# Optimization experiments

Measured on AMD Instinct MI355X. Metric: run time of the kernel, lower is better.

The kernel has to match this reference:

```python
import jax, jax.numpy as jnp
import numpy as np

N, E, G = 200000, 600000, 1024
NF_IN, EF_IN, H = 32, 16, 512
BN_EPS = 1e-5


def _bn(x, gamma, beta):
    # eval-mode BatchNorm1d with running_mean=0, running_var=1
    return x * (gamma / jnp.sqrt(1.0 + BN_EPS)) + beta


def setup_inputs() -> dict:
    key = jax.random.key(0)
    ks = jax.random.split(key, 32)
    s = 0.05
    inp = {
        'nf': jax.random.normal(ks[0], (N, NF_IN), jnp.float32),
        'ef': jax.random.normal(ks[1], (E, EF_IN), jnp.float32),
        'gf': jax.random.normal(ks[2], (G, H), jnp.float32),
        'device_params': jax.random.uniform(ks[3], (N,), jnp.float32),
        'node_y': jax.random.randint(ks[4], (N,), 0, 9),
        'batch_idx': jnp.sort(jax.random.randint(ks[5], (N,), 0, G)),
        'edge_index': jax.random.randint(ks[6], (2, E), 0, N),
        'nf_w1': jax.random.normal(ks[7], (NF_IN + 9, H), jnp.float32) * s,
        'nf_b1': jax.random.normal(ks[8], (H,), jnp.float32) * s,
        'nf_g1': jax.random.uniform(ks[9], (H,), jnp.float32, 0.5, 1.5),
        'nf_be1': jax.random.normal(ks[10], (H,), jnp.float32) * s,
        'nf_w2': jax.random.normal(ks[11], (H, H), jnp.float32) * s,
        'nf_b2': jax.random.normal(ks[12], (H,), jnp.float32) * s,
        'ef_w1': jax.random.normal(ks[13], (EF_IN, H), jnp.float32) * s,
        'ef_b1': jax.random.normal(ks[14], (H,), jnp.float32) * s,
        'ef_g1': jax.random.uniform(ks[15], (H,), jnp.float32, 0.5, 1.5),
        'ef_be1': jax.random.normal(ks[16], (H,), jnp.float32) * s,
        'ef_w2': jax.random.normal(ks[17], (H, H), jnp.float32) * s,
        'ef_b2': jax.random.normal(ks[18], (H,), jnp.float32) * s,
        'ow1': jax.random.normal(ks[19], (H, H), jnp.float32) * s,
        'ob1': jax.random.normal(ks[20], (H,), jnp.float32) * s,
        'og1': jax.random.uniform(ks[21], (H,), jnp.float32, 0.5, 1.5),
        'obe1': jax.random.normal(ks[22], (H,), jnp.float32) * s,
        'ow2': jax.random.normal(ks[23], (H, H), jnp.float32) * s,
        'ob2': jax.random.normal(ks[24], (H,), jnp.float32) * s,
        'og2': jax.random.uniform(ks[25], (H,), jnp.float32, 0.5, 1.5),
        'obe2': jax.random.normal(ks[26], (H,), jnp.float32) * s,
        'ow3': jax.random.normal(ks[27], (H, 2), jnp.float32) * s,
        'ob3': jax.random.normal(ks[28], (2,), jnp.float32) * s,
    }
    return inp


def reference(nf, ef, gf, device_params, node_y, batch_idx, edge_index,
              nf_w1, nf_b1, nf_g1, nf_be1, nf_w2, nf_b2,
              ef_w1, ef_b1, ef_g1, ef_be1, ef_w2, ef_b2,
              ow1, ob1, og1, obe1, ow2, ob2, og2, obe2, ow3, ob3):
    num_graphs = gf.shape[0]
    gelu = lambda x: jax.nn.gelu(x, approximate=False)  # torch nn.GELU default

    # DeviceParam_MLP: augment node features with scaled one-hot of node class
    nf_aug = jnp.concatenate(
        [nf, jax.nn.one_hot(node_y, 9, dtype=nf.dtype) * device_params[:, None]],
        axis=-1)  # [N, nf_in+9]
    h_n = gelu(_bn(nf_aug @ nf_w1 + nf_b1, nf_g1, nf_be1)) @ nf_w2 + nf_b2  # [N,H]
    h_e = gelu(_bn(ef @ ef_w1 + ef_b1, ef_g1, ef_be1)) @ ef_w2 + ef_b2      # [E,H]

    # two scatter_add pools into graph features
    gh = gf
    gh = gh + jax.ops.segment_sum(h_n, batch_idx, num_segments=num_graphs)
    edge_graph = batch_idx[edge_index[0]]  # graph id of each edge's source node
    gh = gh + jax.ops.segment_sum(h_e, edge_graph, num_segments=num_graphs)

    # output MLP (layer_num=3): two hidden blocks + final Linear -> 2
    x = gelu(_bn(gh @ ow1 + ob1, og1, obe1))
    x = gelu(_bn(x @ ow2 + ob2, og2, obe2))
    return x @ ow3 + ob3  # [G, 2]
```

## Files before the change

### kernel.cpp

```cpp
#include <hip/hip_runtime.h>

#define NN 200000
#define NE 600000
#define NG 1024
#define HH 512

typedef short short8 __attribute__((ext_vector_type(8)));
typedef float f32x4 __attribute__((ext_vector_type(4)));
typedef unsigned short ushort_t;

__device__ __forceinline__ unsigned short f2bf(float f){
  unsigned u = __float_as_uint(f);
  u += 0x7fffu + ((u >> 16) & 1u);
  return (unsigned short)(u >> 16);
}
__device__ __forceinline__ float bf2f(unsigned short h){
  return __uint_as_float(((unsigned)h) << 16);
}

__device__ __forceinline__ float gelu_f(float x){
  float p = __builtin_fmaf(x*x, -0.10294325f, -2.3022085f);
  float e = __builtin_amdgcn_exp2f(x * p);
  return x * __builtin_amdgcn_rcpf(1.0f + e);
}

__global__ __launch_bounds__(256) void kpre(
    const float* __restrict__ nfw1, const float* __restrict__ nfb1,
    const float* __restrict__ nfg1, const float* __restrict__ nfbe1,
    const float* __restrict__ efw1, const float* __restrict__ efb1,
    const float* __restrict__ efg1, const float* __restrict__ efbe1,
    unsigned short* __restrict__ w1nT, unsigned short* __restrict__ w1eT,
    float* __restrict__ b1n, float* __restrict__ b1e,
    const int* __restrict__ bidx, int* __restrict__ nstart,
    const int* __restrict__ eidx, int* __restrict__ eg, int* __restrict__ cnte,
    const float* __restrict__ w2n, const float* __restrict__ w2e,
    const float* __restrict__ ow1, const float* __restrict__ ow2,
    ushort_t* __restrict__ bt1h, ushort_t* __restrict__ bt1l,
    ushort_t* __restrict__ bt2h, ushort_t* __restrict__ bt2l,
    ushort_t* __restrict__ bt3h, ushort_t* __restrict__ bt3l){
  __shared__ int h[NG];
  const float rs = 0.99999500003750f;
  int b = blockIdx.x, t = threadIdx.x;
  if (b < 196){
    int tid = b*256 + t;
    if (tid < 512*64){
      int c = tid >> 6, k = tid & 63;
      float w = (k < 41) ? nfw1[k*HH + c] * nfg1[c] * rs : 0.0f;
      w1nT[tid] = f2bf(w);
    } else if (tid < 512*96){
      int u = tid - 512*64; int c = u >> 5, k = u & 31;
      float w = (k < 16) ? efw1[k*HH + c] * efg1[c] * rs : 0.0f;
      w1eT[u] = f2bf(w);
    } else if (tid < 512*96 + 512){
      int c = tid - 512*96;
      b1n[c] = nfb1[c]*nfg1[c]*rs + nfbe1[c];
    } else if (tid < 512*96 + 1024){
      int c = tid - (512*96 + 512);
      b1e[c] = efb1[c]*efg1[c]*rs + efbe1[c];
    }
  } else if (b < 978){
    int i = (b-196)*256 + t;
    if (i < NN){
      int g0 = bidx[i];
      int g1 = (i+1 < NN) ? bidx[i+1] : NG;
      for (int g = g0+1; g <= g1; ++g) nstart[g] = i+1;
      if (i == 0) for (int g = 0; g <= g0; ++g) nstart[g] = 0;
    }
  } else if (b < 1234){
    int hb = b - 978;
    for (int u = t; u < NG; u += 256) h[u] = 0;
    __syncthreads();
    for (int e = hb*256 + t; e < NE; e += 256*256){
      int g = bidx[eidx[e]];
      eg[e] = g;
      atomicAdd(&h[g], 1);
    }
    __syncthreads();
    for (int u = t; u < NG; u += 256){ int c = h[u]; if (c) atomicAdd(&cnte[u], c); }
  } else if (b < 3282){
    int u = (b - 1234)*256 + t;
    int c = u >> 10, k = u & 1023;
    float w = (k < HH) ? w2n[k*HH + c] : w2e[(k-HH)*HH + c];
    unsigned short hh = f2bf(w);
    bt1h[u] = hh;
    bt1l[u] = f2bf(w - bf2f(hh));
  } else if (b < 4306){
    int u = (b - 3282)*256 + t;
    int c = u >> 9, k = u & 511;
    float w = ow1[k*HH + c];
    unsigned short hh = f2bf(w);
    bt2h[u] = hh;
    bt2l[u] = f2bf(w - bf2f(hh));
  } else {
    int u = (b - 4306)*256 + t;
    int c = u >> 9, k = u & 511;
    float w = ow2[k*HH + c];
    unsigned short hh = f2bf(w);
    bt3h[u] = hh;
    bt3l[u] = f2bf(w - bf2f(hh));
  }
}

__global__ __launch_bounds__(1024) void kscan_init(const int* __restrict__ cnte, int* __restrict__ cursor,
    int* __restrict__ estart,
    const float* __restrict__ gf, const int* __restrict__ nstart,
    const float* __restrict__ b2n, const float* __restrict__ b2e,
    float* __restrict__ gh){
  if (blockIdx.x == 0){
    __shared__ int s[NG];
    int t = threadIdx.x;
    int v = cnte[t]; s[t] = v; __syncthreads();
    for (int d = 1; d < NG; d <<= 1){
      int x = (t >= d) ? s[t-d] : 0;
      __syncthreads();
      s[t] += x;
      __syncthreads();
    }
    cursor[t] = s[t] - v;
    estart[t] = s[t] - v;
    if (t == NG-1) estart[NG] = s[t];
  } else {
    int i = (blockIdx.x - 1)*1024 + threadIdx.x;
    int f = i*4;
    int r = f >> 9, c = f & 511;
    float cn = (float)(nstart[r+1] - nstart[r]);
    float ce = (float)cnte[r];
    float4 gv = *(const float4*)&gf[f];
    float4 bn4 = *(const float4*)&b2n[c];
    float4 be4 = *(const float4*)&b2e[c];
    float4 o;
    o.x = gv.x + cn*bn4.x + ce*be4.x;
    o.y = gv.y + cn*bn4.y + ce*be4.y;
    o.z = gv.z + cn*bn4.z + ce*be4.z;
    o.w = gv.w + cn*bn4.w + ce*be4.w;
    *(float4*)&gh[f] = o;
  }
}

__global__ __launch_bounds__(1024) void kscatter(const int* __restrict__ eg, int* __restrict__ cursor,
                                                 int* __restrict__ perm){
  __shared__ int h[NG], base[NG];
  const int per = (NE + gridDim.x - 1) / gridDim.x;
  const int lo = blockIdx.x * per, hi = min(lo + per, NE);
  for (int t = threadIdx.x; t < NG; t += 1024) h[t] = 0;
  __syncthreads();
  for (int e = lo + threadIdx.x; e < hi; e += 1024) atomicAdd(&h[eg[e]], 1);
  __syncthreads();
  for (int t = threadIdx.x; t < NG; t += 1024){
    int c = h[t];
    base[t] = c ? atomicAdd(&cursor[t], c) : 0;
    h[t] = 0;
  }
  __syncthreads();
  for (int e = lo + threadIdx.x; e < hi; e += 1024){
    int g = eg[e];
    int p = base[g] + atomicAdd(&h[g], 1);
    perm[p] = e;
  }
}

__global__ __launch_bounds__(256) void kmain(
    const float* __restrict__ nf, const float* __restrict__ dp, const int* __restrict__ ny,
    const int* __restrict__ nstart, const float* __restrict__ ef, const int* __restrict__ perm,
    const int* __restrict__ estart, const unsigned short* __restrict__ w1nT,
    const unsigned short* __restrict__ w1eT, const float* __restrict__ b1n,
    const float* __restrict__ b1e, float* __restrict__ S){
  const int t = threadIdx.x;
  const int lane = t & 63, w = t >> 6;
  const int q = lane >> 4, m = lane & 15;
  const short8 zz = {0,0,0,0,0,0,0,0};
  if (blockIdx.x < 2048){
    const int g = blockIdx.x >> 1;
    const int c0 = ((blockIdx.x & 1) << 8) + (w << 6);
    short8 bfr[4]; float bias[4]; float colacc[4] = {0.f,0.f,0.f,0.f};
#pragma unroll
    for (int nt=0; nt<4; ++nt){
      int c = c0 + (nt<<4) + m;
      bfr[nt] = *(const short8*)(w1eT + (c << 5) + (q << 3));
      bias[nt] = b1e[c];
    }
    const int s0 = estart[g], s1 = estart[g+1];
    const int nfull = (s1 - s0) >> 4;
    int rb = s0;
    for (int ch=0; ch<nfull; ++ch, rb += 16){
      int e = perm[rb + m];
      short8 f = zz;
      if (q < 2){
        const float4* ap = (const float4*)(ef + (size_t)e*16 + (q<<3));
        float4 xa = ap[0], xb = ap[1];
        f[0]=(short)f2bf(xa.x); f[1]=(short)f2bf(xa.y); f[2]=(short)f2bf(xa.z); f[3]=(short)f2bf(xa.w);
        f[4]=(short)f2bf(xb.x); f[5]=(short)f2bf(xb.y); f[6]=(short)f2bf(xb.z); f[7]=(short)f2bf(xb.w);
      }
#pragma unroll
      for (int nt=0; nt<4; ++nt){
        f32x4 acc = {bias[nt], bias[nt], bias[nt], bias[nt]};
        acc = __builtin_amdgcn_mfma_f32_16x16x32_bf16(f, bfr[nt], acc, 0, 0, 0);
        colacc[nt] += (gelu_f(acc[0]) + gelu_f(acc[1])) + (gelu_f(acc[2]) + gelu_f(acc[3]));
      }
    }
    if (rb < s1){
      int row = rb + m;
      int e = perm[(row < s1) ? row : s0];
      short8 f = zz;
      if (q < 2){
        const float4* ap = (const float4*)(ef + (size_t)e*16 + (q<<3));
        float4 xa = ap[0], xb = ap[1];
        f[0]=(short)f2bf(xa.x); f[1]=(short)f2bf(xa.y); f[2]=(short)f2bf(xa.z); f[3]=(short)f2bf(xa.w);
        f[4]=(short)f2bf(xb.x); f[5]=(short)f2bf(xb.y); f[6]=(short)f2bf(xb.z); f[7]=(short)f2bf(xb.w);
      }
      const int vr = s1 - rb;
#pragma unroll
      for (int nt=0; nt<4; ++nt){
        f32x4 acc = {bias[nt], bias[nt], bias[nt], bias[nt]};
        acc = __builtin_amdgcn_mfma_f32_16x16x32_bf16(f, bfr[nt], acc, 0, 0, 0);
        float v0 = (q*4+0 < vr) ? gelu_f(acc[0]) : 0.f;
        float v1 = (q*4+1 < vr) ? gelu_f(acc[1]) : 0.f;
        float v2 = (q*4+2 < vr) ? gelu_f(acc[2]) : 0.f;
        float v3 = (q*4+3 < vr) ? gelu_f(acc[3]) : 0.f;
        colacc[nt] += (v0+v1)+(v2+v3);
      }
    }
#pragma unroll
    for (int nt=0; nt<4; ++nt){
      float s = colacc[nt];
      s += __shfl_xor(s, 16); s += __shfl_xor(s, 32);
      if (lane < 16) S[(size_t)g*1024 + 512 + c0 + (nt<<4) + lane] = s;
    }
  } else {
    const int b2 = blockIdx.x - 2048;
    const int g = b2 >> 2;
    const int c0 = ((b2 & 3) << 7) + (w << 5);
    short8 bf0[2], bf1[2]; float bias[2]; float colacc[2] = {0.f,0.f};
#pragma unroll
    for (int nt=0; nt<2; ++nt){
      int c = c0 + (nt<<4) + m;
      const short8* bp = (const short8*)(w1nT + (c << 6) + (q << 3));
      bf0[nt] = bp[0]; bf1[nt] = bp[4];
      bias[nt] = b1n[c];
    }
    const int s0 = nstart[g], s1 = nstart[g+1];
    const int nfull = (s1 - s0) >> 4;
    int rb = s0;
    for (int ch=0; ch<nfull; ++ch, rb += 16){
      int ar = rb + m;
      const float4* ap = (const float4*)(nf + (size_t)ar*32 + (q<<3));
      float4 xa = ap[0], xb = ap[1];
      short8 f;
      f[0]=(short)f2bf(xa.x); f[1]=(short)f2bf(xa.y); f[2]=(short)f2bf(xa.z); f[3]=(short)f2bf(xa.w);
      f[4]=(short)f2bf(xb.x); f[5]=(short)f2bf(xb.y); f[6]=(short)f2bf(xb.z); f[7]=(short)f2bf(xb.w);
      int cls = ny[ar];
      short dpb = (short)f2bf(dp[ar]);
      short8 h = zz;
      if (q == 0){
#pragma unroll
        for (int j=0;j<8;++j) h[j] = (cls==j) ? dpb : (short)0;
      } else if (q == 1 && cls == 8) h[0] = dpb;
#pragma unroll
      for (int nt=0; nt<2; ++nt){
        f32x4 acc = {bias[nt], bias[nt], bias[nt], bias[nt]};
        acc = __builtin_amdgcn_mfma_f32_16x16x32_bf16(f, bf0[nt], acc, 0, 0, 0);
        acc = __builtin_amdgcn_mfma_f32_16x16x32_bf16(h, bf1[nt], acc, 0, 0, 0);
        colacc[nt] += (gelu_f(acc[0]) + gelu_f(acc[1])) + (gelu_f(acc[2]) + gelu_f(acc[3]));
      }
    }
    if (rb < s1){
      int row = rb + m;
      int ar = (row < s1) ? row : s0;
      const float4* ap = (const float4*)(nf + (size_t)ar*32 + (q<<3));
      float4 xa = ap[0], xb = ap[1];
      short8 f;
      f[0]=(short)f2bf(xa.x); f[1]=(short)f2bf(xa.y); f[2]=(short)f2bf(xa.z); f[3]=(short)f2bf(xa.w);
      f[4]=(short)f2bf(xb.x); f[5]=(short)f2bf(xb.y); f[6]=(short)f2bf(xb.z); f[7]=(short)f2bf(xb.w);
      int cls = ny[ar];
      short dpb = (short)f2bf(dp[ar]);
      short8 h = zz;
      if (q == 0){
#pragma unroll
        for (int j=0;j<8;++j) h[j] = (cls==j) ? dpb : (short)0;
      } else if (q == 1 && cls == 8) h[0] = dpb;
      const int vr = s1 - rb;
#pragma unroll
      for (int nt=0; nt<2; ++nt){
        f32x4 acc = {bias[nt], bias[nt], bias[nt], bias[nt]};
        acc = __builtin_amdgcn_mfma_f32_16x16x32_bf16(f, bf0[nt], acc, 0, 0, 0);
        acc = __builtin_amdgcn_mfma_f32_16x16x32_bf16(h, bf1[nt], acc, 0, 0, 0);
        float v0 = (q*4+0 < vr) ? gelu_f(acc[0]) : 0.f;
        float v1 = (q*4+1 < vr) ? gelu_f(acc[1]) : 0.f;
        float v2 = (q*4+2 < vr) ? gelu_f(acc[2]) : 0.f;
        float v3 = (q*4+3 < vr) ? gelu_f(acc[3]) : 0.f;
        colacc[nt] += (v0+v1)+(v2+v3);
      }
    }
#pragma unroll
    for (int nt=0; nt<2; ++nt){
      float s = colacc[nt];
      s += __shfl_xor(s, 16); s += __shfl_xor(s, 32);
      if (lane < 16) S[(size_t)g*1024 + c0 + (nt<<4) + lane] = s;
    }
  }
}

__global__ __launch_bounds__(256) void kgemm2(const float* __restrict__ A, int lda, int nkc,
    const ushort_t* __restrict__ bth, const ushort_t* __restrict__ btl, int ldb,
    float* __restrict__ out, const float* __restrict__ pre, const float* __restrict__ bias,
    const float* __restrict__ gam, const float* __restrict__ bet){
  const int t = threadIdx.x, lane = t & 63, w = t >> 6;
  const int q = lane >> 4, m = lane & 15;
  const int c0 = blockIdx.x*32, r0 = blockIdx.y*64 + w*16;
  f32x4 acc[2] = {{0.f,0.f,0.f,0.f},{0.f,0.f,0.f,0.f}};
  const float* ap = A + (size_t)(r0 + m)*lda + (q<<3);
  const ushort_t* bh0 = bth + (size_t)(c0 + m)*ldb + (q<<3);
  const ushort_t* bl0 = btl + (size_t)(c0 + m)*ldb + (q<<3);
  for (int kc = 0; kc < nkc; ++kc){
    const int ko = kc*32;
    float4 x = *(const float4*)(ap + ko);
    float4 y = *(const float4*)(ap + ko + 4);
    float v[8] = {x.x,x.y,x.z,x.w,y.x,y.y,y.z,y.w};
    short8 ah, al;
#pragma unroll
    for (int j=0;j<8;++j){
      unsigned short hh = f2bf(v[j]);
      ah[j] = (short)hh;
      al[j] = (short)f2bf(v[j] - bf2f(hh));
    }
#pragma unroll
    for (int cf=0; cf<2; ++cf){
      short8 bh = *(const short8*)(bh0 + (size_t)(cf*16)*ldb + ko);
      short8 bl = *(const short8*)(bl0 + (size_t)(cf*16)*ldb + ko);
      acc[cf] = __builtin_amdgcn_mfma_f32_16x16x32_bf16(ah, bh, acc[cf], 0, 0, 0);
      acc[cf] = __builtin_amdgcn_mfma_f32_16x16x32_bf16(ah, bl, acc[cf], 0, 0, 0);
      acc[cf] = __builtin_amdgcn_mfma_f32_16x16x32_bf16(al, bh, acc[cf], 0, 0, 0);
    }
  }
  const float rs = 0.99999500003750f;
#pragma unroll
  for (int cf=0; cf<2; ++cf){
    int c = c0 + cf*16 + m;
    float sc = 0.f, bi = 0.f, be = 0.f;
    if (!pre){ sc = gam[c]*rs; bi = bias[c]; be = bet[c]; }
#pragma unroll
    for (int i=0;i<4;++i){
      int r = blockIdx.y*64 + w*16 + q*4 + i;
      float vv = acc[cf][i];
      if (pre) vv += pre[(size_t)r*HH + c];
      else vv = gelu_f((vv + bi)*sc + be);
      out[(size_t)r*HH + c] = vv;
    }
  }
}

__global__ __launch_bounds__(256) void kfinal(const float* __restrict__ x2, const float* __restrict__ w3,
    const float* __restrict__ b3, float* __restrict__ out){
  const int lane = threadIdx.x & 63, wv = threadIdx.x >> 6;
  const int r = blockIdx.x*4 + wv;
  float a0 = 0.f, a1 = 0.f;
#pragma unroll
  for (int tt=0; tt<8; ++tt){
    int k = lane + tt*64;
    float x = x2[(size_t)r*HH + k];
    a0 = __builtin_fmaf(x, w3[2*k], a0);
    a1 = __builtin_fmaf(x, w3[2*k+1], a1);
  }
#pragma unroll
  for (int d=1; d<64; d<<=1){ a0 += __shfl_xor(a0, d); a1 += __shfl_xor(a1, d); }
  if (lane == 0){ out[r*2] = a0 + b3[0]; out[r*2+1] = a1 + b3[1]; }
}

extern "C" void kernel_launch(void* const* d_in, const int* in_sizes, int n_in,
                              void* d_out, int out_size, void* d_ws, size_t ws_size,
                              hipStream_t stream) {
  const float* nf    = (const float*)d_in[0];
  const float* ef    = (const float*)d_in[1];
  const float* gf    = (const float*)d_in[2];
  const float* dp    = (const float*)d_in[3];
  const int*   ny    = (const int*)d_in[4];
  const int*   bidx  = (const int*)d_in[5];
  const int*   eidx  = (const int*)d_in[6];
  const float* nfw1  = (const float*)d_in[7];
  const float* nfb1  = (const float*)d_in[8];
  const float* nfg1  = (const float*)d_in[9];
  const float* nfbe1 = (const float*)d_in[10];
  const float* w2n   = (const float*)d_in[11];
  const float* b2n   = (const float*)d_in[12];
  const float* efw1  = (const float*)d_in[13];
  const float* efb1  = (const float*)d_in[14];
  const float* efg1  = (const float*)d_in[15];
  const float* efbe1 = (const float*)d_in[16];
  const float* w2e   = (const float*)d_in[17];
  const float* b2e   = (const float*)d_in[18];
  const float* ow1   = (const float*)d_in[19];
  const float* ob1   = (const float*)d_in[20];
  const float* og1   = (const float*)d_in[21];
  const float* obe1  = (const float*)d_in[22];
  const float* ow2   = (const float*)d_in[23];
  const float* ob2   = (const float*)d_in[24];
  const float* og2   = (const float*)d_in[25];
  const float* obe2  = (const float*)d_in[26];
  const float* ow3   = (const float*)d_in[27];
  const float* ob3   = (const float*)d_in[28];

  float* S    = (float*)d_ws;
  int* cnte   = (int*)(S + NG*1024);
  int* cursor = cnte + NG;
  int* nstart = cursor + NG;
  int* estart = nstart + NG + 1;
  int* eg     = estart + NG + 1;
  int* perm   = eg + NE;
  unsigned short* w1nT = (unsigned short*)(perm + NE);
  unsigned short* w1eT = w1nT + HH*64;
  float* b1n  = (float*)(w1eT + HH*32);
  float* b1e  = b1n + HH;
  ushort_t* bt1h = (ushort_t*)(b1e + HH);
  ushort_t* bt1l = bt1h + HH*1024;
  ushort_t* bt2h = bt1l + HH*1024;
  ushort_t* bt2l = bt2h + HH*HH;
  ushort_t* bt3h = bt2l + HH*HH;
  ushort_t* bt3l = bt3h + HH*HH;
  float* gh   = (float*)(bt3l + HH*HH);
  float* xg2  = gh + NG*HH;
  float* x2f  = xg2 + NG*HH;

  hipMemsetAsync(cnte, 0, NG*sizeof(int), stream);

  kpre<<<5330, 256, 0, stream>>>(nfw1, nfb1, nfg1, nfbe1, efw1, efb1, efg1, efbe1,
                                 w1nT, w1eT, b1n, b1e, bidx, nstart, eidx, eg, cnte,
                                 w2n, w2e, ow1, ow2, bt1h, bt1l, bt2h, bt2l, bt3h, bt3l);
  kscan_init<<<129, 1024, 0, stream>>>(cnte, cursor, estart, gf, nstart, b2n, b2e, gh);
  kscatter<<<128, 1024, 0, stream>>>(eg, cursor, perm);
  kmain<<<6144, 256, 0, stream>>>(nf, dp, ny, nstart, ef, perm, estart,
                                  w1nT, w1eT, b1n, b1e, S);
  kgemm2<<<dim3(16,16), 256, 0, stream>>>(S, 1024, 32, bt1h, bt1l, 1024, gh, gh,
                                          nullptr, nullptr, nullptr);
  kgemm2<<<dim3(16,16), 256, 0, stream>>>(gh, 512, 16, bt2h, bt2l, 512, xg2, nullptr,
                                          ob1, og1, obe1);
  kgemm2<<<dim3(16,16), 256, 0, stream>>>(xg2, 512, 16, bt3h, bt3l, 512, x2f, nullptr,
                                          ob2, og2, obe2);
  kfinal<<<NG/4, 256, 0, stream>>>(x2f, ow3, ob3, (float*)d_out);
}
```

Measured before the change: 386.5 us.

## Merge preprocessing and tail GEMM kernels into cooperative grid-synced kernels

Replaces the memset, preprocessing, scan/init and scatter kernels with one cooperative kernel of 256 blocks that uses grid.sync between phases. The three tail GEMMs and the final projection are likewise merged into one cooperative kernel. The aim is to cut kernel launch gaps and tail effects across the small dependent stages. In exchange, each front block now handles far more work serially with only 256 blocks, and grid-wide barriers add their own cost.

```diff
diff --git a/kernel.cpp b/kernel.cpp
--- a/kernel.cpp
+++ b/kernel.cpp
@@ -1,4 +1,7 @@
 #include <hip/hip_runtime.h>
+#include <hip/hip_cooperative_groups.h>
+
+namespace cg = cooperative_groups;
 
 #define NN 200000
 #define NE 600000
@@ -24,7 +27,7 @@
   return x * __builtin_amdgcn_rcpf(1.0f + e);
 }
 
-__global__ __launch_bounds__(256) void kpre(
+__global__ __launch_bounds__(256) void kfront(
     const float* __restrict__ nfw1, const float* __restrict__ nfb1,
     const float* __restrict__ nfg1, const float* __restrict__ nfbe1,
     const float* __restrict__ efw1, const float* __restrict__ efb1,
@@ -33,94 +36,107 @@
     float* __restrict__ b1n, float* __restrict__ b1e,
     const int* __restrict__ bidx, int* __restrict__ nstart,
     const int* __restrict__ eidx, int* __restrict__ eg, int* __restrict__ cnte,
+    int* __restrict__ cursor, int* __restrict__ estart, int* __restrict__ perm,
     const float* __restrict__ w2n, const float* __restrict__ w2e,
     const float* __restrict__ ow1, const float* __restrict__ ow2,
     ushort_t* __restrict__ bt1h, ushort_t* __restrict__ bt1l,
     ushort_t* __restrict__ bt2h, ushort_t* __restrict__ bt2l,
-    ushort_t* __restrict__ bt3h, ushort_t* __restrict__ bt3l){
+    ushort_t* __restrict__ bt3h, ushort_t* __restrict__ bt3l,
+    const float* __restrict__ gf, const float* __restrict__ b2n, const float* __restrict__ b2e,
+    float* __restrict__ gh){
   __shared__ int h[NG];
+  __shared__ int aux[NG];
+  cg::grid_group grid = cg::this_grid();
   const float rs = 0.99999500003750f;
-  int b = blockIdx.x, t = threadIdx.x;
-  if (b < 196){
-    int tid = b*256 + t;
-    if (tid < 512*64){
-      int c = tid >> 6, k = tid & 63;
-      float w = (k < 41) ? nfw1[k*HH + c] * nfg1[c] * rs : 0.0f;
-      w1nT[tid] = f2bf(w);
-    } else if (tid < 512*96){
-      int u = tid - 512*64; int c = u >> 5, k = u & 31;
-      float w = (k < 16) ? efw1[k*HH + c] * efg1[c] * rs : 0.0f;
-      w1eT[u] = f2bf(w);
-    } else if (tid < 512*96 + 512){
-      int c = tid - 512*96;
-      b1n[c] = nfb1[c]*nfg1[c]*rs + nfbe1[c];
-    } else if (tid < 512*96 + 1024){
-      int c = tid - (512*96 + 512);
-      b1e[c] = efb1[c]*efg1[c]*rs + efbe1[c];
-    }
-  } else if (b < 978){
-    int i = (b-196)*256 + t;
-    if (i < NN){
-      int g0 = bidx[i];
-      int g1 = (i+1 < NN) ? bidx[i+1] : NG;
-      for (int g = g0+1; g <= g1; ++g) nstart[g] = i+1;
-      if (i == 0) for (int g = 0; g <= g0; ++g) nstart[g] = 0;
-    }
-  } else if (b < 1234){
-    int hb = b - 978;
-    for (int u = t; u < NG; u += 256) h[u] = 0;
-    __syncthreads();
-    for (int e = hb*256 + t; e < NE; e += 256*256){
-      int g = bidx[eidx[e]];
-      eg[e] = g;
-      atomicAdd(&h[g], 1);
-    }
-    __syncthreads();
-    for (int u = t; u < NG; u += 256){ int c = h[u]; if (c) atomicAdd(&cnte[u], c); }
-  } else if (b < 3282){
-    int u = (b - 1234)*256 + t;
+  const int b = blockIdx.x, t = threadIdx.x;
+  const int gtid = b*256 + t;
+
+  if (gtid < NG) cnte[gtid] = 0;
+  if (gtid < 512*64){
+    int c = gtid >> 6, k = gtid & 63;
+    float w = (k < 41) ? nfw1[k*HH + c] * nfg1[c] * rs : 0.0f;
+    w1nT[gtid] = f2bf(w);
+  } else if (gtid < 512*96){
+    int u = gtid - 512*64; int c = u >> 5, k = u & 31;
+    float w = (k < 16) ? efw1[k*HH + c] * efg1[c] * rs : 0.0f;
+    w1eT[u] = f2bf(w);
+  } else if (gtid < 512*96 + 512){
+    int c = gtid - 512*96;
+    b1n[c] = nfb1[c]*nfg1[c]*rs + nfbe1[c];
+  } else if (gtid < 512*96 + 1024){
+    int c = gtid - (512*96 + 512);
+    b1e[c] = efb1[c]*efg1[c]*rs + efbe1[c];
+  }
+  for (int u = gtid; u < 512*1024; u += 65536){
     int c = u >> 10, k = u & 1023;
     float w = (k < HH) ? w2n[k*HH + c] : w2e[(k-HH)*HH + c];
     unsigned short hh = f2bf(w);
-    bt1h[u] = hh;
-    bt1l[u] = f2bf(w - bf2f(hh));
-  } else if (b < 4306){
-    int u = (b - 3282)*256 + t;
+    bt1h[u] = hh; bt1l[u] = f2bf(w - bf2f(hh));
+  }
+  for (int u = gtid; u < 512*512; u += 65536){
     int c = u >> 9, k = u & 511;
     float w = ow1[k*HH + c];
     unsigned short hh = f2bf(w);
-    bt2h[u] = hh;
-    bt2l[u] = f2bf(w - bf2f(hh));
-  } else {
-    int u = (b - 4306)*256 + t;
+    bt2h[u] = hh; bt2l[u] = f2bf(w - bf2f(hh));
+  }
+  for (int u = gtid; u < 512*512; u += 65536){
     int c = u >> 9, k = u & 511;
     float w = ow2[k*HH + c];
     unsigned short hh = f2bf(w);
-    bt3h[u] = hh;
-    bt3l[u] = f2bf(w - bf2f(hh));
-  }
-}
-
-__global__ __launch_bounds__(1024) void kscan_init(const int* __restrict__ cnte, int* __restrict__ cursor,
-    int* __restrict__ estart,
-    const float* __restrict__ gf, const int* __restrict__ nstart,
-    const float* __restrict__ b2n, const float* __restrict__ b2e,
-    float* __restrict__ gh){
-  if (blockIdx.x == 0){
-    __shared__ int s[NG];
-    int t = threadIdx.x;
-    int v = cnte[t]; s[t] = v; __syncthreads();
-    for (int d = 1; d < NG; d <<= 1){
-      int x = (t >= d) ? s[t-d] : 0;
+    bt3h[u] = hh; bt3l[u] = f2bf(w - bf2f(hh));
+  }
+  for (int i = gtid; i < NN; i += 65536){
+    int g0 = bidx[i];
+    int g1 = (i+1 < NN) ? bidx[i+1] : NG;
+    for (int g = g0+1; g <= g1; ++g) nstart[g] = i+1;
+    if (i == 0) for (int g = 0; g <= g0; ++g) nstart[g] = 0;
+  }
+  for (int u = t; u < NG; u += 256) h[u] = 0;
+  __syncthreads();
+  const int per = (NE + 255) / 256;
+  const int lo = b*per, hi = min(lo + per, NE);
+  for (int e = lo + t; e < hi; e += 256){
+    int g = bidx[eidx[e]];
+    eg[e] = g;
+    atomicAdd(&h[g], 1);
+  }
+  grid.sync();
+
+  for (int u = t; u < NG; u += 256){ int c = h[u]; if (c) atomicAdd(&cnte[u], c); }
+  grid.sync();
+
+  if (b == 0){
+    int v0 = cnte[t*4], v1 = cnte[t*4+1], v2 = cnte[t*4+2], v3 = cnte[t*4+3];
+    int s4 = v0+v1+v2+v3;
+    aux[t] = s4;
+    __syncthreads();
+    for (int d = 1; d < 256; d <<= 1){
+      int x = (t >= d) ? aux[t-d] : 0;
       __syncthreads();
-      s[t] += x;
+      aux[t] += x;
       __syncthreads();
     }
-    cursor[t] = s[t] - v;
-    estart[t] = s[t] - v;
-    if (t == NG-1) estart[NG] = s[t];
-  } else {
-    int i = (blockIdx.x - 1)*1024 + threadIdx.x;
+    int b0 = aux[t] - s4;
+    estart[t*4]   = b0;           cursor[t*4]   = b0;
+    estart[t*4+1] = b0+v0;        cursor[t*4+1] = b0+v0;
+    estart[t*4+2] = b0+v0+v1;     cursor[t*4+2] = b0+v0+v1;
+    estart[t*4+3] = b0+v0+v1+v2;  cursor[t*4+3] = b0+v0+v1+v2;
+    if (t == 255) estart[NG] = aux[255];
+  }
+  grid.sync();
+
+  for (int u = t; u < NG; u += 256){
+    int c = h[u];
+    aux[u] = c ? atomicAdd(&cursor[u], c) : 0;
+    h[u] = 0;
+  }
+  __syncthreads();
+  for (int e = lo + t; e < hi; e += 256){
+    int g = eg[e];
+    int p = aux[g] + atomicAdd(&h[g], 1);
+    perm[p] = e;
+  }
+  for (int i = gtid; i < NG*HH/4; i += 65536){
     int f = i*4;
     int r = f >> 9, c = f & 511;
     float cn = (float)(nstart[r+1] - nstart[r]);
@@ -134,28 +150,6 @@
     o.z = gv.z + cn*bn4.z + ce*be4.z;
     o.w = gv.w + cn*bn4.w + ce*be4.w;
     *(float4*)&gh[f] = o;
-  }
-}
-
-__global__ __launch_bounds__(1024) void kscatter(const int* __restrict__ eg, int* __restrict__ cursor,
-                                                 int* __restrict__ perm){
-  __shared__ int h[NG], base[NG];
-  const int per = (NE + gridDim.x - 1) / gridDim.x;
-  const int lo = blockIdx.x * per, hi = min(lo + per, NE);
-  for (int t = threadIdx.x; t < NG; t += 1024) h[t] = 0;
-  __syncthreads();
-  for (int e = lo + threadIdx.x; e < hi; e += 1024) atomicAdd(&h[eg[e]], 1);
-  __syncthreads();
-  for (int t = threadIdx.x; t < NG; t += 1024){
-    int c = h[t];
-    base[t] = c ? atomicAdd(&cursor[t], c) : 0;
-    h[t] = 0;
-  }
-  __syncthreads();
-  for (int e = lo + threadIdx.x; e < hi; e += 1024){
-    int g = eg[e];
-    int p = base[g] + atomicAdd(&h[g], 1);
-    perm[p] = e;
   }
 }
 
@@ -300,13 +294,14 @@
   }
 }
 
-__global__ __launch_bounds__(256) void kgemm2(const float* __restrict__ A, int lda, int nkc,
+__device__ __forceinline__ void gemm_nolds(int cx, int ry,
+    const float* __restrict__ A, int lda, int nkc,
     const ushort_t* __restrict__ bth, const ushort_t* __restrict__ btl, int ldb,
     float* __restrict__ out, const float* __restrict__ pre, const float* __restrict__ bias,
     const float* __restrict__ gam, const float* __restrict__ bet){
   const int t = threadIdx.x, lane = t & 63, w = t >> 6;
   const int q = lane >> 4, m = lane & 15;
-  const int c0 = blockIdx.x*32, r0 = blockIdx.y*64 + w*16;
+  const int c0 = cx*32, r0 = ry*64 + w*16;
   f32x4 acc[2] = {{0.f,0.f,0.f,0.f},{0.f,0.f,0.f,0.f}};
   const float* ap = A + (size_t)(r0 + m)*lda + (q<<3);
   const ushort_t* bh0 = bth + (size_t)(c0 + m)*ldb + (q<<3);
@@ -340,7 +335,7 @@
     if (!pre){ sc = gam[c]*rs; bi = bias[c]; be = bet[c]; }
 #pragma unroll
     for (int i=0;i<4;++i){
-      int r = blockIdx.y*64 + w*16 + q*4 + i;
+      int r = ry*64 + w*16 + q*4 + i;
       float vv = acc[cf][i];
       if (pre) vv += pre[(size_t)r*HH + c];
       else vv = gelu_f((vv + bi)*sc + be);
@@ -349,21 +344,37 @@
   }
 }
 
-__global__ __launch_bounds__(256) void kfinal(const float* __restrict__ x2, const float* __restrict__ w3,
-    const float* __restrict__ b3, float* __restrict__ out){
+__global__ __launch_bounds__(256) void kback(
+    const float* __restrict__ S,
+    const ushort_t* __restrict__ bt1h, const ushort_t* __restrict__ bt1l, float* __restrict__ gh,
+    const ushort_t* __restrict__ bt2h, const ushort_t* __restrict__ bt2l,
+    const float* __restrict__ ob1, const float* __restrict__ og1, const float* __restrict__ obe1,
+    float* __restrict__ xg2,
+    const ushort_t* __restrict__ bt3h, const ushort_t* __restrict__ bt3l,
+    const float* __restrict__ ob2, const float* __restrict__ og2, const float* __restrict__ obe2,
+    float* __restrict__ x2f,
+    const float* __restrict__ ow3, const float* __restrict__ ob3, float* __restrict__ out){
+  cg::grid_group grid = cg::this_grid();
+  const int cx = blockIdx.x & 15, ry = blockIdx.x >> 4;
+  gemm_nolds(cx, ry, S, 1024, 32, bt1h, bt1l, 1024, gh, gh, nullptr, nullptr, nullptr);
+  grid.sync();
+  gemm_nolds(cx, ry, gh, 512, 16, bt2h, bt2l, 512, xg2, nullptr, ob1, og1, obe1);
+  grid.sync();
+  gemm_nolds(cx, ry, xg2, 512, 16, bt3h, bt3l, 512, x2f, nullptr, ob2, og2, obe2);
+  grid.sync();
   const int lane = threadIdx.x & 63, wv = threadIdx.x >> 6;
   const int r = blockIdx.x*4 + wv;
   float a0 = 0.f, a1 = 0.f;
 #pragma unroll
   for (int tt=0; tt<8; ++tt){
     int k = lane + tt*64;
-    float x = x2[(size_t)r*HH + k];
-    a0 = __builtin_fmaf(x, w3[2*k], a0);
-    a1 = __builtin_fmaf(x, w3[2*k+1], a1);
+    float x = x2f[(size_t)r*HH + k];
+    a0 = __builtin_fmaf(x, ow3[2*k], a0);
+    a1 = __builtin_fmaf(x, ow3[2*k+1], a1);
   }
 #pragma unroll
   for (int d=1; d<64; d<<=1){ a0 += __shfl_xor(a0, d); a1 += __shfl_xor(a1, d); }
-  if (lane == 0){ out[r*2] = a0 + b3[0]; out[r*2+1] = a1 + b3[1]; }
+  if (lane == 0){ out[r*2] = a0 + ob3[0]; out[r*2+1] = a1 + ob3[1]; }
 }
 
 extern "C" void kernel_launch(void* const* d_in, const int* in_sizes, int n_in,
@@ -419,21 +430,27 @@
   float* gh   = (float*)(bt3l + HH*HH);
   float* xg2  = gh + NG*HH;
   float* x2f  = xg2 + NG*HH;
-
-  hipMemsetAsync(cnte, 0, NG*sizeof(int), stream);
-
-  kpre<<<5330, 256, 0, stream>>>(nfw1, nfb1, nfg1, nfbe1, efw1, efb1, efg1, efbe1,
-                                 w1nT, w1eT, b1n, b1e, bidx, nstart, eidx, eg, cnte,
-                                 w2n, w2e, ow1, ow2, bt1h, bt1l, bt2h, bt2l, bt3h, bt3l);
-  kscan_init<<<129, 1024, 0, stream>>>(cnte, cursor, estart, gf, nstart, b2n, b2e, gh);
-  kscatter<<<128, 1024, 0, stream>>>(eg, cursor, perm);
+  float* outf = (float*)d_out;
+
+  void* fargs[] = { (void*)&nfw1, (void*)&nfb1, (void*)&nfg1, (void*)&nfbe1,
+                    (void*)&efw1, (void*)&efb1, (void*)&efg1, (void*)&efbe1,
+                    (void*)&w1nT, (void*)&w1eT, (void*)&b1n, (void*)&b1e,
+                    (void*)&bidx, (void*)&nstart, (void*)&eidx, (void*)&eg, (void*)&cnte,
+                    (void*)&cursor, (void*)&estart, (void*)&perm,
+                    (void*)&w2n, (void*)&w2e, (void*)&ow1, (void*)&ow2,
+                    (void*)&bt1h, (void*)&bt1l, (void*)&bt2h, (void*)&bt2l,
+                    (void*)&bt3h, (void*)&bt3l,
+                    (void*)&gf, (void*)&b2n, (void*)&b2e, (void*)&gh };
+  hipLaunchCooperativeKernel((void*)kfront, dim3(256), dim3(256), fargs, 0, stream);
+
   kmain<<<6144, 256, 0, stream>>>(nf, dp, ny, nstart, ef, perm, estart,
                                   w1nT, w1eT, b1n, b1e, S);
-  kgemm2<<<dim3(16,16), 256, 0, stream>>>(S, 1024, 32, bt1h, bt1l, 1024, gh, gh,
-                                          nullptr, nullptr, nullptr);
-  kgemm2<<<dim3(16,16), 256, 0, stream>>>(gh, 512, 16, bt2h, bt2l, 512, xg2, nullptr,
-                                          ob1, og1, obe1);
-  kgemm2<<<dim3(16,16), 256, 0, stream>>>(xg2, 512, 16, bt3h, bt3l, 512, x2f, nullptr,
-                                          ob2, og2, obe2);
-  kfinal<<<NG/4, 256, 0, stream>>>(x2f, ow3, ob3, (float*)d_out);
-}
+
+  void* bargs[] = { (void*)&S, (void*)&bt1h, (void*)&bt1l, (void*)&gh,
+                    (void*)&bt2h, (void*)&bt2l, (void*)&ob1, (void*)&og1, (void*)&obe1,
+                    (void*)&xg2,
+                    (void*)&bt3h, (void*)&bt3l, (void*)&ob2, (void*)&og2, (void*)&obe2,
+                    (void*)&x2f,
+                    (void*)&ow3, (void*)&ob3, (void*)&outf };
+  hipLaunchCooperativeKernel((void*)kback, dim3(256), dim3(256), bargs, 0, stream);
+}
```

Measured after the change: 593.9 us. 1.54x slower.
